# Kernel optimization log

Hardware: AMD Instinct MI355X
Metric: run time of the kernel (lower is better)

## Reference

```python
import jax, jax.numpy as jnp
import numpy as np

B, S, E, H = 1, 2048, 2048, 32
D = E // H  # head_dim = 64
QMAX = 127.0


def _ste(x, xq):
    # straight-through fake quant (forward = xq, grad = identity)
    return x + jax.lax.stop_gradient(xq - x)


def fake_quant_act(x):
    # per-tensor symmetric int8 fake quantization (QuantMatMul.quant_x*/act quantizer)
    scale = jnp.maximum(jnp.max(jnp.abs(x)) / QMAX, 1e-8)
    xq = jnp.clip(jnp.round(x / scale), -128.0, QMAX) * scale
    return _ste(x, xq)


def fake_quant_weight(w):
    # per-output-channel symmetric int8 fake quantization (weight quantizer)
    scale = jnp.maximum(jnp.max(jnp.abs(w), axis=1, keepdims=True) / QMAX, 1e-8)
    wq = jnp.clip(jnp.round(w / scale), -128.0, QMAX) * scale
    return _ste(w, wq)


def rope_cos_sin(seq_len, dim):
    inv_freq = 1.0 / (10000.0 ** (jnp.arange(0, dim, 2, dtype=jnp.float32) / dim))
    t = jnp.arange(seq_len, dtype=jnp.float32)
    freqs = jnp.outer(t, inv_freq)            # [S, D/2]
    emb = jnp.concatenate([freqs, freqs], -1)  # [S, D]
    return jnp.cos(emb), jnp.sin(emb)


def rotate_half(x):
    x1, x2 = jnp.split(x, 2, axis=-1)
    return jnp.concatenate([-x2, x1], axis=-1)


def setup_inputs() -> dict:
    key = jax.random.key(0)
    ks = jax.random.split(key, 5)
    return {
        "hidden_states": jax.random.normal(ks[0], (B, S, E), dtype=jnp.float32),
        "w_q": jax.random.normal(ks[1], (E, E), dtype=jnp.float32) * 0.02,
        "w_k": jax.random.normal(ks[2], (E, E), dtype=jnp.float32) * 0.02,
        "w_v": jax.random.normal(ks[3], (E, E), dtype=jnp.float32) * 0.02,
        "w_o": jax.random.normal(ks[4], (E, E), dtype=jnp.float32) * 0.02,
    }


def reference(hidden_states, w_q, w_k, w_v, w_o):
    scaling = D ** -0.5
    # quantized projections (QuantLinear: fake-quant weight, no input quant for q/k/v)
    q = hidden_states @ fake_quant_weight(w_q).T * scaling
    k = hidden_states @ fake_quant_weight(w_k).T
    v = hidden_states @ fake_quant_weight(w_v).T
    # qkt_matmul.quant_x1/quant_x2, pv_matmul.quant_x2
    q = fake_quant_act(q)
    k = fake_quant_act(k)
    v = fake_quant_act(v)
    # [B,S,E] -> [B,H,S,D]
    q = q.reshape(B, S, H, D).transpose(0, 2, 1, 3)
    k = k.reshape(B, S, H, D).transpose(0, 2, 1, 3)
    v = v.reshape(B, S, H, D).transpose(0, 2, 1, 3)
    # rotary embedding
    cos, sin = rope_cos_sin(S, D)
    cos = cos[None, None]
    sin = sin[None, None]
    q = q * cos + rotate_half(q) * sin
    k = k * cos + rotate_half(k) * sin
    # QK^T (already scaled via q) + causal mask
    scores = jnp.einsum("bhsd,bhtd->bhst", q, k)  # [B,H,S,S]
    causal = jnp.tril(jnp.ones((S, S), dtype=bool))
    scores = jnp.where(causal[None, None], scores, jnp.finfo(scores.dtype).min)
    probs = jax.nn.softmax(scores.astype(jnp.float32), axis=-1).astype(q.dtype)
    # PV matmul (v already fake-quantized)
    out = jnp.einsum("bhst,bhtd->bhsd", probs, v)
    out = out.transpose(0, 2, 1, 3).reshape(B, S, E)
    # o_proj: QuantLinear with input quant enabled
    out = fake_quant_act(out) @ fake_quant_weight(w_o).T
    return out
```

## Files before the change

### kernel.cpp

```cpp
#include <hip/hip_runtime.h>
#include <hip/hip_bf16.h>
#include <hip/hip_fp16.h>

#define S_LEN 2048
#define E_DIM 2048
#define H_NUM 32
#define D_DIM 64

typedef __attribute__((ext_vector_type(8))) short short8;
typedef __attribute__((ext_vector_type(4))) short short4v;
typedef __attribute__((ext_vector_type(4))) float f32x4;
typedef __attribute__((ext_vector_type(4))) int i32x4;

__device__ __forceinline__ unsigned short f2h(float f) {
  return __builtin_bit_cast(unsigned short, (_Float16)f);
}

__device__ __forceinline__ float h2f(unsigned short u) {
  return (float)__builtin_bit_cast(_Float16, u);
}

__device__ __forceinline__ float fq1(float x, float invs, float scale) {
  return fminf(fmaxf(rintf(x * invs), -128.f), 127.f) * scale;
}

__device__ __forceinline__ int q8(float x, float invs) {
  return min(max((int)rintf(x * invs), -128), 127);
}

__device__ __forceinline__ void gload_lds16(const void* g, void* l) {
  __builtin_amdgcn_global_load_lds((const __attribute__((address_space(1))) void*)g,
                                   (__attribute__((address_space(3))) void*)l, 16, 0, 0);
}

__device__ __forceinline__ f32x4 mfma16h(short8 a, short8 b, f32x4 c) {
  return __builtin_amdgcn_mfma_f32_16x16x32_f16(a, b, c, 0, 0, 0);
}

__device__ __forceinline__ i32x4 mfma16i8(i32x4 a, i32x4 b, i32x4 c) {
  return __builtin_amdgcn_mfma_i32_16x16x64_i8(a, b, c, 0, 0, 0);
}

#define VMW4() asm volatile("s_waitcnt vmcnt(4)" ::: "memory")
#define VMW3() asm volatile("s_waitcnt vmcnt(3)" ::: "memory")
#define VMW0() asm volatile("s_waitcnt vmcnt(0)" ::: "memory")
#define BARR() asm volatile("s_barrier" ::: "memory")
#define LGKM0() asm volatile("s_waitcnt lgkmcnt(0)" ::: "memory")

__global__ void k_prep(const float* __restrict__ hs,
                       const float* __restrict__ w_q, const float* __restrict__ w_k,
                       const float* __restrict__ w_v, const float* __restrict__ w_o,
                       unsigned short* __restrict__ hsb, unsigned short* __restrict__ wq_all,
                       signed char* __restrict__ wo_i8, float* __restrict__ wsc,
                       unsigned* __restrict__ sc, float2* __restrict__ trig) {
  const int b = blockIdx.x;
  if (b < 4096) {
    int i = b * 256 + threadIdx.x;
    float4 v = ((const float4*)hs)[i];
    ushort4 r;
    r.x = f2h(v.x); r.y = f2h(v.y); r.z = f2h(v.z); r.w = f2h(v.w);
    ((ushort4*)hsb)[i] = r;
    return;
  }
  if (b >= 12288) {
    if (b == 12288) {
      if (threadIdx.x < 8) sc[threadIdx.x] = 0u;
      return;
    }
    int idx = (b - 12289) * 256 + threadIdx.x;
    int s = idx >> 5, i = idx & 31;
    float freq = exp2f(-(float)i * (13.287712379549449f / 32.f));
    float ang = (float)s * freq;
    float sn, cs;
    sincosf(ang, &sn, &cs);
    float2 t; t.x = cs; t.y = sn;
    trig[idx] = t;
    return;
  }
  __shared__ float wm[4];
  const int isWo = (b >= 10240);
  const int bb = isWo ? (b - 10240) : (b - 4096);
  const int wy = isWo ? 0 : (bb >> 11);
  const int wx = isWo ? bb : (bb & 2047);
  const float* w = isWo ? w_o : (wy == 0 ? w_q : wy == 1 ? w_k : w_v);
  const float* row = w + (size_t)wx * E_DIM;
  float4 a = ((const float4*)row)[threadIdx.x * 2];
  float4 bq = ((const float4*)row)[threadIdx.x * 2 + 1];
  float m = fmaxf(fmaxf(fmaxf(fabsf(a.x), fabsf(a.y)), fmaxf(fabsf(a.z), fabsf(a.w))),
                  fmaxf(fmaxf(fabsf(bq.x), fabsf(bq.y)), fmaxf(fabsf(bq.z), fabsf(bq.w))));
#pragma unroll
  for (int off = 32; off; off >>= 1) m = fmaxf(m, __shfl_xor(m, off));
  if ((threadIdx.x & 63) == 0) wm[threadIdx.x >> 6] = m;
  __syncthreads();
  m = fmaxf(fmaxf(wm[0], wm[1]), fmaxf(wm[2], wm[3]));
  float scale = fmaxf(m * (1.f / 127.f), 1e-8f);
  float invs = 1.f / scale;
  if (isWo) {
    unsigned lo = (unsigned)(q8(a.x, invs) & 255) | ((unsigned)(q8(a.y, invs) & 255) << 8) |
                  ((unsigned)(q8(a.z, invs) & 255) << 16) | ((unsigned)(q8(a.w, invs) & 255) << 24);
    unsigned hi = (unsigned)(q8(bq.x, invs) & 255) | ((unsigned)(q8(bq.y, invs) & 255) << 8) |
                  ((unsigned)(q8(bq.z, invs) & 255) << 16) | ((unsigned)(q8(bq.w, invs) & 255) << 24);
    uint2 pk; pk.x = lo; pk.y = hi;
    ((uint2*)(wo_i8 + (size_t)wx * E_DIM))[threadIdx.x] = pk;
    if (threadIdx.x == 0) wsc[wx] = scale;
  } else {
    unsigned short* orow = wq_all + (size_t)wy * E_DIM * E_DIM + (size_t)wx * E_DIM;
    ushort4 r0, r1;
    r0.x = f2h(fq1(a.x, invs, scale)); r0.y = f2h(fq1(a.y, invs, scale));
    r0.z = f2h(fq1(a.z, invs, scale)); r0.w = f2h(fq1(a.w, invs, scale));
    r1.x = f2h(fq1(bq.x, invs, scale)); r1.y = f2h(fq1(bq.y, invs, scale));
    r1.z = f2h(fq1(bq.z, invs, scale)); r1.w = f2h(fq1(bq.w, invs, scale));
    ((ushort4*)orow)[threadIdx.x * 2] = r0;
    ((ushort4*)orow)[threadIdx.x * 2 + 1] = r1;
  }
}

__global__ __launch_bounds__(512, 2)
void k_gemm_qkv(const unsigned short* __restrict__ A, const unsigned short* __restrict__ Bt,
                unsigned short* __restrict__ C, unsigned* __restrict__ amax, float alpha_q) {
  __shared__ char lds[131072];
  const int K = 2048, NT = 32;
  const int lin = blockIdx.x;
  const int swz = (lin & 7) * 24 + (lin >> 3);
  const int z = swz >> 6;
  const int t64 = swz & 63;
  const int iby = t64 >> 3;
  const int ibx = t64 & 7;
  const unsigned short* Bz = Bt + (size_t)z * E_DIM * E_DIM;
  unsigned short* Cz = C + (size_t)z * S_LEN * E_DIM;
  const float alpha = (z == 0) ? alpha_q : 1.0f;

  const int tid = threadIdx.x;
  const int wv = tid >> 6, ln = tid & 63;
  const int wm = wv >> 2, wn = wv & 3;
  const size_t bm = (size_t)ibx * 256, bn = (size_t)iby * 256;
  const int arow = ln & 15, gsl = ln >> 4;

  int abyte[8], bbyte[4];
#pragma unroll
  for (int i = 0; i < 8; ++i) {
    int r = wm * 128 + i * 16 + arow;
    abyte[i] = r * 64 + ((gsl ^ ((r >> 1) & 3)) * 16);
  }
#pragma unroll
  for (int j = 0; j < 4; ++j) {
    int r = wn * 64 + j * 16 + arow;
    bbyte[j] = 32768 + r * 64 + ((gsl ^ ((r >> 1) & 3)) * 16);
  }

  const int srow = tid >> 2;
  const int scc = (tid & 3) ^ ((tid >> 3) & 3);
  const unsigned short* Asrc = A + (bm + srow) * (size_t)K + scc * 8;
  const unsigned short* Bsrc = Bz + (bn + srow) * (size_t)K + scc * 8;
  const int ldst = tid * 16;

#define STGA(T, S) do { \
    char* d_ = lds + ((T) & 1) * 65536 + (S) * 16384 + ldst; \
    const unsigned short* s_ = Asrc + (T) * 64 + (S) * 32; \
    gload_lds16(s_, d_); \
    gload_lds16(s_ + (size_t)128 * K, d_ + 8192); } while (0)
#define STGB(T, S) do { \
    char* d_ = lds + ((T) & 1) * 65536 + 32768 + (S) * 16384 + ldst; \
    const unsigned short* s_ = Bsrc + (T) * 64 + (S) * 32; \
    gload_lds16(s_, d_); \
    gload_lds16(s_ + (size_t)128 * K, d_ + 8192); } while (0)

  f32x4 acc[8][4];
#pragma unroll
  for (int i = 0; i < 8; ++i)
#pragma unroll
    for (int j = 0; j < 4; ++j) { acc[i][j][0] = 0.f; acc[i][j][1] = 0.f; acc[i][j][2] = 0.f; acc[i][j][3] = 0.f; }

  STGA(0, 0); STGB(0, 0); STGA(0, 1); STGB(0, 1);
  VMW4();
  BARR();

#define TILE(BUF, DS, T1, W2X, W4X) do { \
    char* bp_ = lds + (BUF); \
    short8 af_[8], bf_[4]; \
     \
    _Pragma("unroll") for (int i = 0; i < 8; ++i) af_[i] = *(const short8*)(bp_ + abyte[i]); \
    _Pragma("unroll") for (int j = 0; j < 4; ++j) bf_[j] = *(const short8*)(bp_ + bbyte[j]); \
    if (DS) { STGA(T1, 0); STGB(T1, 0); } \
    LGKM0(); \
    __builtin_amdgcn_s_setprio(1); \
    _Pragma("unroll") for (int i = 0; i < 8; ++i) \
      _Pragma("unroll") for (int j = 0; j < 4; ++j) acc[i][j] = mfma16h(af_[i], bf_[j], acc[i][j]); \
    __builtin_amdgcn_s_setprio(0); \
    W2X; \
    BARR(); \
     \
    _Pragma("unroll") for (int i = 0; i < 8; ++i) af_[i] = *(const short8*)(bp_ + 16384 + abyte[i]); \
    _Pragma("unroll") for (int j = 0; j < 4; ++j) bf_[j] = *(const short8*)(bp_ + 16384 + bbyte[j]); \
    if (DS) { STGA(T1, 1); STGB(T1, 1); } \
    LGKM0(); \
    __builtin_amdgcn_s_setprio(1); \
    _Pragma("unroll") for (int i = 0; i < 8; ++i) \
      _Pragma("unroll") for (int j = 0; j < 4; ++j) acc[i][j] = mfma16h(af_[i], bf_[j], acc[i][j]); \
    __builtin_amdgcn_s_setprio(0); \
    W4X; \
    BARR(); \
  } while (0)

#pragma unroll 1
  for (int t = 0; t < NT - 2; t += 2) {
    TILE(0, 1, t + 1, VMW4(), VMW4());
    TILE(65536, 1, t + 2, VMW4(), VMW4());
  }
  TILE(0, 1, NT - 1, VMW4(), VMW4());
  TILE(65536, 0, 0, VMW0(), (void)0);
#undef TILE
#undef STGA
#undef STGB

  float amx = 0.f;
#pragma unroll
  for (int i = 0; i < 8; ++i) {
    size_t rowb = bm + wm * 128 + i * 16 + gsl * 4;
#pragma unroll
    for (int j = 0; j < 4; ++j) {
      size_t col = bn + wn * 64 + j * 16 + arow;
#pragma unroll
      for (int r = 0; r < 4; ++r) {
        float v = acc[i][j][r] * alpha;
        Cz[(rowb + r) * E_DIM + col] = f2h(v);
        amx = fmaxf(amx, fabsf(v));
      }
    }
  }
#pragma unroll
  for (int off = 32; off; off >>= 1) amx = fmaxf(amx, __shfl_xor(amx, off));
  if (ln == 0) atomicMax(amax + z, __float_as_uint(amx));
}

__global__ __launch_bounds__(256, 4)
void k_gemm_o(const signed char* __restrict__ A, const signed char* __restrict__ Bt,
              float* __restrict__ C, const unsigned* __restrict__ sc,
              const float* __restrict__ wsc) {
  __shared__ char lds[36864];
  const int K = 2048, NT = 32;
  const float sa = fmaxf(__uint_as_float(sc[3]) * (1.f / 127.f), 1e-8f);
  const int lin = blockIdx.y * 16 + blockIdx.x;
  const int swz = (lin & 7) * 64 + (lin >> 3);
  const int iby = swz >> 4;
  const int ibx = swz & 15;

  const int tid = threadIdx.x;
  const int wv = tid >> 6, ln = tid & 63;
  const int wm = wv >> 1, wn = wv & 1;
  const size_t bm = (size_t)ibx * 128, bn = (size_t)iby * 64;
  const int arow = ln & 15, gsl = ln >> 4;

  int abyte[4], bbyte[2];
#pragma unroll
  for (int i = 0; i < 4; ++i) {
    int ra = wm * 64 + i * 16 + arow;
    abyte[i] = ra * 64 + ((gsl ^ ((ra >> 1) & 3)) * 16);
  }
#pragma unroll
  for (int j = 0; j < 2; ++j) {
    int rb = wn * 32 + j * 16 + arow;
    bbyte[j] = rb * 64 + ((gsl ^ ((rb >> 1) & 3)) * 16);
  }

  const int srow = tid >> 2;
  const int sl = (tid & 3) ^ ((srow >> 1) & 3);
  const signed char* Ast = A + (bm + srow) * (size_t)K + sl * 16;
  const signed char* Bst = Bt + (bn + srow) * (size_t)K + sl * 16;

#define STG(T, dst) do { if ((T) < NT) { \
    size_t go = (size_t)(T) * 64; \
    gload_lds16(Ast + go, (dst) + wv * 1024); \
    gload_lds16(Ast + go + (size_t)64 * K, (dst) + 4096 + wv * 1024); \
    gload_lds16(Bst + go, (dst) + 8192 + wv * 1024); } } while (0)

  i32x4 acc[4][2];
#pragma unroll
  for (int i = 0; i < 4; ++i)
#pragma unroll
    for (int j = 0; j < 2; ++j) { acc[i][j][0] = 0; acc[i][j][1] = 0; acc[i][j][2] = 0; acc[i][j][3] = 0; }

  char* b0 = lds;
  char* b1 = lds + 12288;
  char* b2 = lds + 24576;

  STG(0, b0); STG(1, b1);
  VMW3();
  BARR();

#define ITER(T, bufR, bufS) do { \
    i32x4 af[4], bf[2]; \
    _Pragma("unroll") \
    for (int i = 0; i < 4; ++i) af[i] = *(const i32x4*)((bufR) + abyte[i]); \
    _Pragma("unroll") \
    for (int j = 0; j < 2; ++j) bf[j] = *(const i32x4*)((bufR) + 8192 + bbyte[j]); \
    STG((T) + 2, bufS); \
    __builtin_amdgcn_s_setprio(1); \
    _Pragma("unroll") \
    for (int i = 0; i < 4; ++i) \
      _Pragma("unroll") \
      for (int j = 0; j < 2; ++j) acc[i][j] = mfma16i8(af[i], bf[j], acc[i][j]); \
    __builtin_amdgcn_s_setprio(0); \
    if ((T) == NT - 2) { VMW0(); } else if ((T) < NT - 2) { VMW3(); } \
    BARR(); } while (0)

#pragma unroll 1
  for (int t = 0; t + 2 < NT; t += 3) {
    ITER(t, b0, b2);
    ITER(t + 1, b1, b0);
    ITER(t + 2, b2, b1);
  }
  ITER(NT - 2, b0, b2);
  ITER(NT - 1, b1, b0);
#undef ITER
#undef STG

#pragma unroll
  for (int i = 0; i < 4; ++i) {
    size_t rowb = bm + wm * 64 + i * 16 + gsl * 4;
#pragma unroll
    for (int j = 0; j < 2; ++j) {
      size_t col = bn + wn * 32 + j * 16 + arow;
      float s = sa * wsc[col];
#pragma unroll
      for (int r = 0; r < 4; ++r)
        C[(rowb + r) * E_DIM + col] = (float)acc[i][j][r] * s;
    }
  }
}

__global__ void k_rvt(const unsigned short* __restrict__ qkv,
                      unsigned short* __restrict__ Qh, unsigned short* __restrict__ Kh,
                      unsigned short* __restrict__ Vt, const unsigned* __restrict__ sc,
                      const float2* __restrict__ trig) {
  __shared__ float tb[64][65];
  const int z = blockIdx.z;
  if (z < 2) {
    const unsigned short* x = qkv + (z ? 4194304 : 0);
    unsigned short* out = z ? Kh : Qh;
    float scale = fmaxf(__uint_as_float(sc[z]) * (1.f / 127.f), 1e-8f);
    float invs = 1.f / scale;
    const int h = blockIdx.y;
    const int tid = threadIdx.x;
    const int s = blockIdx.x * 32 + (tid >> 3);
    const int j = tid & 7;
    short8 v = *(const short8*)(x + (size_t)s * E_DIM + h * 64 + j * 8);
    int pi[4];
    {
      const int* vi = (const int*)&v;
#pragma unroll
      for (int w = 0; w < 4; ++w) pi[w] = __shfl_xor(vi[w], 4);
    }
    short8 p = *(const short8*)pi;
    const float sgn = (j < 4) ? -1.f : 1.f;
    const float2* tp = trig + s * 32 + (j & 3) * 8;
    short8 ro;
#pragma unroll
    for (int e = 0; e < 8; ++e) {
      float me = fq1(h2f((unsigned short)v[e]), invs, scale);
      float pe = fq1(h2f((unsigned short)p[e]), invs, scale);
      float2 t = tp[e];
      ro[e] = (short)f2h(me * t.x + sgn * (pe * t.y));
    }
    *(short8*)(out + (size_t)h * S_LEN * D_DIM + (size_t)s * D_DIM + j * 8) = ro;
    return;
  }
  if (blockIdx.x >= 32) return;
  const unsigned short* v = qkv + 2 * 4194304;
  float scale = fmaxf(__uint_as_float(sc[2]) * (1.f / 127.f), 1e-8f);
  float invs = 1.f / scale;
  int s0 = blockIdx.x * 64, h = blockIdx.y;
#pragma unroll
  for (int l = 0; l < 16; ++l) {
    int idx = threadIdx.x + l * 256;
    int r = idx >> 6, c = idx & 63;
    float x = h2f(v[(size_t)(s0 + r) * E_DIM + h * 64 + c]);
    tb[r][c] = fq1(x, invs, scale);
  }
  __syncthreads();
#pragma unroll
  for (int l = 0; l < 16; ++l) {
    int idx = threadIdx.x + l * 256;
    int d = idx >> 6, s = idx & 63;
    Vt[(size_t)h * D_DIM * S_LEN + (size_t)d * S_LEN + s0 + s] = f2h(tb[s][d]);
  }
}

__global__ __launch_bounds__(256, 4)
void k_attn(const unsigned short* __restrict__ Qh, const unsigned short* __restrict__ Kh,
            const unsigned short* __restrict__ Vt, unsigned short* __restrict__ att,
            unsigned* __restrict__ amax) {
  __shared__ char Kbuf[2 * 8192];
  __shared__ char Vbuf[2 * 8192];
  __shared__ __align__(16) char Pb[8192];
  const int L = blockIdx.x;
  const int h = L & 31;
  const int g = L >> 5;
  const int p = g & 7, gg = g >> 3;
  const int qc = (gg == 0) ? (31 - p) : (gg == 1) ? p : (gg == 2) ? (23 - p) : (8 + p);
  const int nt = qc + 1;
  const int tid = threadIdx.x;
  const int wv = tid >> 6, ln = tid & 63;
  const int arow = ln & 15, gsl = ln >> 4;
  const unsigned short* Qb = Qh + (size_t)h * S_LEN * D_DIM;
  const unsigned short* Kb = Kh + (size_t)h * S_LEN * D_DIM;
  const unsigned short* Vb = Vt + (size_t)h * D_DIM * S_LEN;
  const int qr = qc * 64 + wv * 16;

  const int srow0 = tid >> 3, sch0 = (tid & 7) ^ (srow0 & 7);
  const int srow1 = 32 + (tid >> 3), sch1 = (tid & 7) ^ (srow1 & 7);

#define STAGEK(T, B) do { char* kd = Kbuf + (B) * 8192; const int tb_ = (T) * 64; \
    gload_lds16(Kb + (size_t)(tb_ + srow0) * D_DIM + sch0 * 8, kd + wv * 1024); \
    gload_lds16(Kb + (size_t)(tb_ + srow1) * D_DIM + sch1 * 8, kd + 4096 + wv * 1024); } while (0)
#define STAGEV(T, B) do { char* vd = Vbuf + (B) * 8192; const int tb_ = (T) * 64; \
    gload_lds16(Vb + (size_t)srow0 * S_LEN + tb_ + sch0 * 8, vd + wv * 1024); \
    gload_lds16(Vb + (size_t)srow1 * S_LEN + tb_ + sch1 * 8, vd + 4096 + wv * 1024); } while (0)

  short8 qa0 = *(const short8*)(Qb + (size_t)(qr + arow) * D_DIM + gsl * 8);
  short8 qa1 = *(const short8*)(Qb + (size_t)(qr + arow) * D_DIM + 32 + gsl * 8);

  f32x4 o[4];
  float mrow = -INFINITY, lrow = 0.f;
#pragma unroll
  for (int d = 0; d < 4; ++d) { o[d][0] = 0.f; o[d][1] = 0.f; o[d][2] = 0.f; o[d][3] = 0.f; }

  STAGEK(0, 0);
  STAGEV(0, 0);
  if (nt > 1) { STAGEK(1, 1); STAGEV(1, 1); VMW4(); } else { VMW0(); }
  BARR();

  char* Pw = Pb + wv * 2048 + arow * 128;
  const int arw7 = arow & 7;

#pragma unroll 1
  for (int t = 0; t < nt; ++t) {
    if (t >= 1 && t + 1 < nt) { STAGEK(t + 1, (t + 1) & 1); STAGEV(t + 1, (t + 1) & 1); }
    char* kb = Kbuf + (t & 1) * 8192;
    char* vb = Vbuf + (t & 1) * 8192;

    short8 kf[4][2];
#pragma unroll
    for (int kvb = 0; kvb < 4; ++kvb) {
      int row = kvb * 16 + arow;
      int sw = (row & 7) << 4;
      kf[kvb][0] = *(const short8*)(kb + row * 128 + ((gsl * 16) ^ sw));
      kf[kvb][1] = *(const short8*)(kb + row * 128 + ((64 + gsl * 16) ^ sw));
    }
    f32x4 s4[4];
#pragma unroll
    for (int kvb = 0; kvb < 4; ++kvb) {
      s4[kvb][0] = 0.f; s4[kvb][1] = 0.f; s4[kvb][2] = 0.f; s4[kvb][3] = 0.f;
    }
#pragma unroll
    for (int kvb = 0; kvb < 4; ++kvb) {
      s4[kvb] = mfma16h(kf[kvb][0], qa0, s4[kvb]);
      s4[kvb] = mfma16h(kf[kvb][1], qa1, s4[kvb]);
    }

    const int t0 = t * 64;
    const int qrow = qr + arow;
    if (t0 + 63 > qrow) {
#pragma unroll
      for (int kvb = 0; kvb < 4; ++kvb) {
        int colb = t0 + kvb * 16 + gsl * 4;
#pragma unroll
        for (int r = 0; r < 4; ++r)
          if (colb + r > qrow) s4[kvb][r] = -INFINITY;
      }
    }

    float smax = s4[0][0];
#pragma unroll
    for (int kvb = 0; kvb < 4; ++kvb)
#pragma unroll
      for (int r = 0; r < 4; ++r) smax = fmaxf(smax, s4[kvb][r]);
    smax = fmaxf(smax, __shfl_xor(smax, 16));
    smax = fmaxf(smax, __shfl_xor(smax, 32));

    float mn = fmaxf(mrow, smax);
    float corr = __expf(mrow - mn);
    mrow = mn;

    float rs = 0.f;
    float p4[4][4];
#pragma unroll
    for (int kvb = 0; kvb < 4; ++kvb)
#pragma unroll
      for (int r = 0; r < 4; ++r) {
        p4[kvb][r] = __expf(s4[kvb][r] - mn);
        rs += p4[kvb][r];
      }
    rs += __shfl_xor(rs, 16);
    rs += __shfl_xor(rs, 32);
    lrow = lrow * corr + rs;

    float corr_r[4];
#pragma unroll
    for (int r = 0; r < 4; ++r) corr_r[r] = __shfl(corr, gsl * 4 + r);
#pragma unroll
    for (int d = 0; d < 4; ++d)
#pragma unroll
      for (int r = 0; r < 4; ++r) o[d][r] *= corr_r[r];

    __builtin_amdgcn_wave_barrier();
#pragma unroll
    for (int kvb = 0; kvb < 4; ++kvb) {
      short4v pw;
      pw[0] = (short)f2h(p4[kvb][0]);
      pw[1] = (short)f2h(p4[kvb][1]);
      pw[2] = (short)f2h(p4[kvb][2]);
      pw[3] = (short)f2h(p4[kvb][3]);
      const int u = kvb * 2 + (gsl >> 1);
      *(short4v*)(Pw + ((u ^ arw7) << 4) + ((gsl & 1) << 3)) = pw;
    }
    __builtin_amdgcn_wave_barrier();
    short8 pa0 = *(const short8*)(Pw + ((gsl ^ arw7) << 4));
    short8 pa1 = *(const short8*)(Pw + (((4 + gsl) ^ arw7) << 4));
    __builtin_amdgcn_wave_barrier();

    short8 vf[4][2];
#pragma unroll
    for (int d = 0; d < 4; ++d) {
      int row = d * 16 + arow;
      int sw = (row & 7) << 4;
      vf[d][0] = *(const short8*)(vb + row * 128 + ((gsl * 16) ^ sw));
      vf[d][1] = *(const short8*)(vb + row * 128 + ((64 + gsl * 16) ^ sw));
    }
#pragma unroll
    for (int d = 0; d < 4; ++d) {
      o[d] = mfma16h(pa0, vf[d][0], o[d]);
      o[d] = mfma16h(pa1, vf[d][1], o[d]);
    }

    VMW0();
    BARR();
  }
#undef STAGEK
#undef STAGEV

  float amx = 0.f;
  float invl = 1.f / lrow;
  float invl_r[4];
#pragma unroll
  for (int r = 0; r < 4; ++r) invl_r[r] = __shfl(invl, gsl * 4 + r);
#pragma unroll
  for (int r = 0; r < 4; ++r) {
    size_t row = (size_t)(qr + gsl * 4 + r);
#pragma unroll
    for (int d = 0; d < 4; ++d) {
      float v = o[d][r] * invl_r[r];
      att[row * E_DIM + h * 64 + d * 16 + arow] = f2h(v);
      amx = fmaxf(amx, fabsf(v));
    }
  }

#pragma unroll
  for (int off = 32; off; off >>= 1) amx = fmaxf(amx, __shfl_xor(amx, off));
  if (ln == 0) atomicMax(amax + 3, __float_as_uint(amx));
}

__global__ void k_quant_act_i8(const unsigned short* __restrict__ in, uint2* __restrict__ out,
                               const unsigned* __restrict__ sc, int idx) {
  float scale = fmaxf(__uint_as_float(sc[idx]) * (1.f / 127.f), 1e-8f);
  float invs = 1.f / scale;
  int i = blockIdx.x * blockDim.x + threadIdx.x;
  short8 v = ((const short8*)in)[i];
  unsigned lo = 0, hi = 0;
#pragma unroll
  for (int e = 0; e < 4; ++e)
    lo |= (unsigned)(q8(h2f((unsigned short)v[e]), invs) & 255) << (8 * e);
#pragma unroll
  for (int e = 0; e < 4; ++e)
    hi |= (unsigned)(q8(h2f((unsigned short)v[4 + e]), invs) & 255) << (8 * e);
  uint2 pk; pk.x = lo; pk.y = hi;
  out[i] = pk;
}

extern "C" void kernel_launch(void* const* d_in, const int* in_sizes, int n_in,
                              void* d_out, int out_size, void* d_ws, size_t ws_size,
                              hipStream_t stream) {
  const float* hs = (const float*)d_in[0];
  const float* w_q = (const float*)d_in[1];
  const float* w_k = (const float*)d_in[2];
  const float* w_v = (const float*)d_in[3];
  const float* w_o = (const float*)d_in[4];

  char* ws = (char*)d_ws;
  unsigned short* wq_all = (unsigned short*)(ws);
  signed char* wo_i8 = (signed char*)(ws + 25165824);
  float* wsc = (float*)(ws + 29360128);
  float2* trig = (float2*)(ws + 30408704);
  unsigned short* hsb = (unsigned short*)(ws + 33554432);
  unsigned short* qkv16 = (unsigned short*)(ws + 41943040);
  unsigned short* att = qkv16;
  signed char* aq_i8 = (signed char*)(ws + 67108864);
  unsigned short* Qh = (unsigned short*)(ws + 92274688);
  unsigned short* Kh = (unsigned short*)(ws + 100663296);
  unsigned short* Vt = (unsigned short*)(ws + 109051904);
  unsigned* sc = (unsigned*)(ws + 117440512);

  k_prep<<<12545, 256, 0, stream>>>(hs, w_q, w_k, w_v, w_o, hsb, wq_all, wo_i8, wsc, sc, trig);
  k_gemm_qkv<<<dim3(192), 512, 0, stream>>>(hsb, wq_all, qkv16, sc, 0.125f);
  k_rvt<<<dim3(64, 32, 3), 256, 0, stream>>>(qkv16, Qh, Kh, Vt, sc, trig);
  k_attn<<<1024, 256, 0, stream>>>(Qh, Kh, Vt, att, sc);
  k_quant_act_i8<<<2048, 256, 0, stream>>>(att, (uint2*)aq_i8, sc, 3);
  k_gemm_o<<<dim3(16, 32), 256, 0, stream>>>(aq_i8, wo_i8, (float*)d_out, sc, wsc);
}
```

Baseline: 183.6 us.

## Process two 64-row query chunks per attention block to reuse K/V tiles

Each attention workgroup now handles a 128-row query tile as two 64-row groups that share every staged K/V tile, halving the grid to 512 blocks. This cuts global-to-LDS traffic and the number of K/V staging barriers per unit of work. The cost is doubled accumulator and Q registers, so launch bounds drop to 2 waves per SIMD. The grid is also smaller and the longest block is twice as long, which may hurt load balance and occupancy.

```diff
diff --git a/kernel.cpp b/kernel.cpp
--- a/kernel.cpp
+++ b/kernel.cpp
@@ -386,7 +386,7 @@
   }
 }
 
-__global__ __launch_bounds__(256, 4)
+__global__ __launch_bounds__(256, 2)
 void k_attn(const unsigned short* __restrict__ Qh, const unsigned short* __restrict__ Kh,
             const unsigned short* __restrict__ Vt, unsigned short* __restrict__ att,
             unsigned* __restrict__ amax) {
@@ -395,17 +395,17 @@
   __shared__ __align__(16) char Pb[8192];
   const int L = blockIdx.x;
   const int h = L & 31;
-  const int g = L >> 5;
-  const int p = g & 7, gg = g >> 3;
-  const int qc = (gg == 0) ? (31 - p) : (gg == 1) ? p : (gg == 2) ? (23 - p) : (8 + p);
-  const int nt = qc + 1;
+  const int g5 = L >> 5;
+  const int qc = (g5 < 8) ? (15 - g5) : (g5 - 8);
+  const int nt = 2 * qc + 2;
   const int tid = threadIdx.x;
   const int wv = tid >> 6, ln = tid & 63;
   const int arow = ln & 15, gsl = ln >> 4;
   const unsigned short* Qb = Qh + (size_t)h * S_LEN * D_DIM;
   const unsigned short* Kb = Kh + (size_t)h * S_LEN * D_DIM;
   const unsigned short* Vb = Vt + (size_t)h * D_DIM * S_LEN;
-  const int qr = qc * 64 + wv * 16;
+  const int qr0 = qc * 128 + wv * 16;
+  const int qr1 = qr0 + 64;
 
   const int srow0 = tid >> 3, sch0 = (tid & 7) ^ (srow0 & 7);
   const int srow1 = 32 + (tid >> 3), sch1 = (tid & 7) ^ (srow1 & 7);
@@ -417,17 +417,25 @@
     gload_lds16(Vb + (size_t)srow0 * S_LEN + tb_ + sch0 * 8, vd + wv * 1024); \
     gload_lds16(Vb + (size_t)srow1 * S_LEN + tb_ + sch1 * 8, vd + 4096 + wv * 1024); } while (0)
 
-  short8 qa0 = *(const short8*)(Qb + (size_t)(qr + arow) * D_DIM + gsl * 8);
-  short8 qa1 = *(const short8*)(Qb + (size_t)(qr + arow) * D_DIM + 32 + gsl * 8);
-
-  f32x4 o[4];
-  float mrow = -INFINITY, lrow = 0.f;
-#pragma unroll
-  for (int d = 0; d < 4; ++d) { o[d][0] = 0.f; o[d][1] = 0.f; o[d][2] = 0.f; o[d][3] = 0.f; }
+  short8 qa[2][2];
+  qa[0][0] = *(const short8*)(Qb + (size_t)(qr0 + arow) * D_DIM + gsl * 8);
+  qa[0][1] = *(const short8*)(Qb + (size_t)(qr0 + arow) * D_DIM + 32 + gsl * 8);
+  qa[1][0] = *(const short8*)(Qb + (size_t)(qr1 + arow) * D_DIM + gsl * 8);
+  qa[1][1] = *(const short8*)(Qb + (size_t)(qr1 + arow) * D_DIM + 32 + gsl * 8);
+
+  f32x4 o[2][4];
+  float mrow[2], lrow[2];
+#pragma unroll
+  for (int gq = 0; gq < 2; ++gq) {
+    mrow[gq] = -INFINITY; lrow[gq] = 0.f;
+#pragma unroll
+    for (int d = 0; d < 4; ++d) { o[gq][d][0] = 0.f; o[gq][d][1] = 0.f; o[gq][d][2] = 0.f; o[gq][d][3] = 0.f; }
+  }
 
   STAGEK(0, 0);
   STAGEV(0, 0);
-  if (nt > 1) { STAGEK(1, 1); STAGEV(1, 1); VMW4(); } else { VMW0(); }
+  STAGEK(1, 1); STAGEV(1, 1);
+  VMW4();
   BARR();
 
   char* Pw = Pb + wv * 2048 + arow * 128;
@@ -447,78 +455,6 @@
       kf[kvb][0] = *(const short8*)(kb + row * 128 + ((gsl * 16) ^ sw));
       kf[kvb][1] = *(const short8*)(kb + row * 128 + ((64 + gsl * 16) ^ sw));
     }
-    f32x4 s4[4];
-#pragma unroll
-    for (int kvb = 0; kvb < 4; ++kvb) {
-      s4[kvb][0] = 0.f; s4[kvb][1] = 0.f; s4[kvb][2] = 0.f; s4[kvb][3] = 0.f;
-    }
-#pragma unroll
-    for (int kvb = 0; kvb < 4; ++kvb) {
-      s4[kvb] = mfma16h(kf[kvb][0], qa0, s4[kvb]);
-      s4[kvb] = mfma16h(kf[kvb][1], qa1, s4[kvb]);
-    }
-
-    const int t0 = t * 64;
-    const int qrow = qr + arow;
-    if (t0 + 63 > qrow) {
-#pragma unroll
-      for (int kvb = 0; kvb < 4; ++kvb) {
-        int colb = t0 + kvb * 16 + gsl * 4;
-#pragma unroll
-        for (int r = 0; r < 4; ++r)
-          if (colb + r > qrow) s4[kvb][r] = -INFINITY;
-      }
-    }
-
-    float smax = s4[0][0];
-#pragma unroll
-    for (int kvb = 0; kvb < 4; ++kvb)
-#pragma unroll
-      for (int r = 0; r < 4; ++r) smax = fmaxf(smax, s4[kvb][r]);
-    smax = fmaxf(smax, __shfl_xor(smax, 16));
-    smax = fmaxf(smax, __shfl_xor(smax, 32));
-
-    float mn = fmaxf(mrow, smax);
-    float corr = __expf(mrow - mn);
-    mrow = mn;
-
-    float rs = 0.f;
-    float p4[4][4];
-#pragma unroll
-    for (int kvb = 0; kvb < 4; ++kvb)
-#pragma unroll
-      for (int r = 0; r < 4; ++r) {
-        p4[kvb][r] = __expf(s4[kvb][r] - mn);
-        rs += p4[kvb][r];
-      }
-    rs += __shfl_xor(rs, 16);
-    rs += __shfl_xor(rs, 32);
-    lrow = lrow * corr + rs;
-
-    float corr_r[4];
-#pragma unroll
-    for (int r = 0; r < 4; ++r) corr_r[r] = __shfl(corr, gsl * 4 + r);
-#pragma unroll
-    for (int d = 0; d < 4; ++d)
-#pragma unroll
-      for (int r = 0; r < 4; ++r) o[d][r] *= corr_r[r];
-
-    __builtin_amdgcn_wave_barrier();
-#pragma unroll
-    for (int kvb = 0; kvb < 4; ++kvb) {
-      short4v pw;
-      pw[0] = (short)f2h(p4[kvb][0]);
-      pw[1] = (short)f2h(p4[kvb][1]);
-      pw[2] = (short)f2h(p4[kvb][2]);
-      pw[3] = (short)f2h(p4[kvb][3]);
-      const int u = kvb * 2 + (gsl >> 1);
-      *(short4v*)(Pw + ((u ^ arw7) << 4) + ((gsl & 1) << 3)) = pw;
-    }
-    __builtin_amdgcn_wave_barrier();
-    short8 pa0 = *(const short8*)(Pw + ((gsl ^ arw7) << 4));
-    short8 pa1 = *(const short8*)(Pw + (((4 + gsl) ^ arw7) << 4));
-    __builtin_amdgcn_wave_barrier();
-
     short8 vf[4][2];
 #pragma unroll
     for (int d = 0; d < 4; ++d) {
@@ -527,10 +463,90 @@
       vf[d][0] = *(const short8*)(vb + row * 128 + ((gsl * 16) ^ sw));
       vf[d][1] = *(const short8*)(vb + row * 128 + ((64 + gsl * 16) ^ sw));
     }
-#pragma unroll
-    for (int d = 0; d < 4; ++d) {
-      o[d] = mfma16h(pa0, vf[d][0], o[d]);
-      o[d] = mfma16h(pa1, vf[d][1], o[d]);
+
+    const int t0 = t * 64;
+
+#pragma unroll
+    for (int gq = 0; gq < 2; ++gq) {
+      if (gq == 0 && t == nt - 1) continue;
+      const int qrg = (gq == 0) ? qr0 : qr1;
+
+      f32x4 s4[4];
+#pragma unroll
+      for (int kvb = 0; kvb < 4; ++kvb) {
+        s4[kvb][0] = 0.f; s4[kvb][1] = 0.f; s4[kvb][2] = 0.f; s4[kvb][3] = 0.f;
+      }
+#pragma unroll
+      for (int kvb = 0; kvb < 4; ++kvb) {
+        s4[kvb] = mfma16h(kf[kvb][0], qa[gq][0], s4[kvb]);
+        s4[kvb] = mfma16h(kf[kvb][1], qa[gq][1], s4[kvb]);
+      }
+
+      const int qrow = qrg + arow;
+      if (t0 + 63 > qrow) {
+#pragma unroll
+        for (int kvb = 0; kvb < 4; ++kvb) {
+          int colb = t0 + kvb * 16 + gsl * 4;
+#pragma unroll
+          for (int r = 0; r < 4; ++r)
+            if (colb + r > qrow) s4[kvb][r] = -INFINITY;
+        }
+      }
+
+      float smax = s4[0][0];
+#pragma unroll
+      for (int kvb = 0; kvb < 4; ++kvb)
+#pragma unroll
+        for (int r = 0; r < 4; ++r) smax = fmaxf(smax, s4[kvb][r]);
+      smax = fmaxf(smax, __shfl_xor(smax, 16));
+      smax = fmaxf(smax, __shfl_xor(smax, 32));
+
+      float mn = fmaxf(mrow[gq], smax);
+      float corr = __expf(mrow[gq] - mn);
+      mrow[gq] = mn;
+
+      float rs = 0.f;
+      float p4[4][4];
+#pragma unroll
+      for (int kvb = 0; kvb < 4; ++kvb)
+#pragma unroll
+        for (int r = 0; r < 4; ++r) {
+          p4[kvb][r] = __expf(s4[kvb][r] - mn);
+          rs += p4[kvb][r];
+        }
+      rs += __shfl_xor(rs, 16);
+      rs += __shfl_xor(rs, 32);
+      lrow[gq] = lrow[gq] * corr + rs;
+
+      float corr_r[4];
+#pragma unroll
+      for (int r = 0; r < 4; ++r) corr_r[r] = __shfl(corr, gsl * 4 + r);
+#pragma unroll
+      for (int d = 0; d < 4; ++d)
+#pragma unroll
+        for (int r = 0; r < 4; ++r) o[gq][d][r] *= corr_r[r];
+
+      __builtin_amdgcn_wave_barrier();
+#pragma unroll
+      for (int kvb = 0; kvb < 4; ++kvb) {
+        short4v pw;
+        pw[0] = (short)f2h(p4[kvb][0]);
+        pw[1] = (short)f2h(p4[kvb][1]);
+        pw[2] = (short)f2h(p4[kvb][2]);
+        pw[3] = (short)f2h(p4[kvb][3]);
+        const int u = kvb * 2 + (gsl >> 1);
+        *(short4v*)(Pw + ((u ^ arw7) << 4) + ((gsl & 1) << 3)) = pw;
+      }
+      __builtin_amdgcn_wave_barrier();
+      short8 pa0 = *(const short8*)(Pw + ((gsl ^ arw7) << 4));
+      short8 pa1 = *(const short8*)(Pw + (((4 + gsl) ^ arw7) << 4));
+      __builtin_amdgcn_wave_barrier();
+
+#pragma unroll
+      for (int d = 0; d < 4; ++d) {
+        o[gq][d] = mfma16h(pa0, vf[d][0], o[gq][d]);
+        o[gq][d] = mfma16h(pa1, vf[d][1], o[gq][d]);
+      }
     }
 
     VMW0();
@@ -540,18 +556,22 @@
 #undef STAGEV
 
   float amx = 0.f;
-  float invl = 1.f / lrow;
-  float invl_r[4];
-#pragma unroll
-  for (int r = 0; r < 4; ++r) invl_r[r] = __shfl(invl, gsl * 4 + r);
-#pragma unroll
-  for (int r = 0; r < 4; ++r) {
-    size_t row = (size_t)(qr + gsl * 4 + r);
-#pragma unroll
-    for (int d = 0; d < 4; ++d) {
-      float v = o[d][r] * invl_r[r];
-      att[row * E_DIM + h * 64 + d * 16 + arow] = f2h(v);
-      amx = fmaxf(amx, fabsf(v));
+#pragma unroll
+  for (int gq = 0; gq < 2; ++gq) {
+    const int qrg = (gq == 0) ? qr0 : qr1;
+    float invl = 1.f / lrow[gq];
+    float invl_r[4];
+#pragma unroll
+    for (int r = 0; r < 4; ++r) invl_r[r] = __shfl(invl, gsl * 4 + r);
+#pragma unroll
+    for (int r = 0; r < 4; ++r) {
+      size_t row = (size_t)(qrg + gsl * 4 + r);
+#pragma unroll
+      for (int d = 0; d < 4; ++d) {
+        float v = o[gq][d][r] * invl_r[r];
+        att[row * E_DIM + h * 64 + d * 16 + arow] = f2h(v);
+        amx = fmaxf(amx, fabsf(v));
+      }
     }
   }
 
@@ -603,7 +623,7 @@
   k_prep<<<12545, 256, 0, stream>>>(hs, w_q, w_k, w_v, w_o, hsb, wq_all, wo_i8, wsc, sc, trig);
   k_gemm_qkv<<<dim3(192), 512, 0, stream>>>(hsb, wq_all, qkv16, sc, 0.125f);
   k_rvt<<<dim3(64, 32, 3), 256, 0, stream>>>(qkv16, Qh, Kh, Vt, sc, trig);
-  k_attn<<<1024, 256, 0, stream>>>(Qh, Kh, Vt, att, sc);
+  k_attn<<<512, 256, 0, stream>>>(Qh, Kh, Vt, att, sc);
   k_quant_act_i8<<<2048, 256, 0, stream>>>(att, (uint2*)aq_i8, sc, 3);
   k_gemm_o<<<dim3(16, 32), 256, 0, stream>>>(aq_i8, wo_i8, (float*)d_out, sc, wsc);
 }
```

Result: faster. 177.2 us (-3.5%).
